# Optimization experiments

Measured on AMD Instinct MI355X. Metric: run time of the kernel, lower is better.

The kernel has to match this reference:

```python
import jax, jax.numpy as jnp
import numpy as np

N_EMBD = 1024
N_HEAD = 16
HEAD_DIM = N_EMBD // N_HEAD


def setup_inputs() -> dict:
    key = jax.random.key(0)
    ks = jax.random.split(key, 5)
    x = jax.random.normal(ks[0], (2, 2048, N_EMBD), dtype=jnp.float32)
    # Linear params, scaled like torch default init (~U(-1/sqrt(fan_in),..)) approximated with small normal
    s = 1.0 / np.sqrt(N_EMBD)
    W_qkv = jax.random.normal(ks[1], (N_EMBD, 3 * N_EMBD), dtype=jnp.float32) * s
    b_qkv = jax.random.normal(ks[2], (3 * N_EMBD,), dtype=jnp.float32) * s
    W_proj = jax.random.normal(ks[3], (N_EMBD, N_EMBD), dtype=jnp.float32) * s
    b_proj = jax.random.normal(ks[4], (N_EMBD,), dtype=jnp.float32) * s
    return {"x": x, "W_qkv": W_qkv, "b_qkv": b_qkv, "W_proj": W_proj, "b_proj": b_proj}


def reference(x, W_qkv, b_qkv, W_proj, b_proj):
    B, T, C = x.shape
    qkv = x @ W_qkv + b_qkv                              # [B,T,3C]
    qkv = qkv.reshape(B, T, 3, N_HEAD, HEAD_DIM)
    qkv = jnp.transpose(qkv, (2, 0, 3, 1, 4))            # [3,B,H,T,D]
    q, k, v = qkv[0], qkv[1], qkv[2]
    scale = HEAD_DIM ** -0.5
    att = jnp.einsum('bhqd,bhkd->bhqk', q, k) * scale    # [B,H,T,T]
    causal = jnp.tril(jnp.ones((T, T), dtype=bool))
    att = jnp.where(causal, att, -jnp.inf)
    att = jax.nn.softmax(att, axis=-1)
    y = jnp.einsum('bhqk,bhkd->bhqd', att, v)            # [B,H,T,D]
    y = jnp.transpose(y, (0, 2, 1, 3)).reshape(B, T, C)
    return y @ W_proj + b_proj
```

## Files before the change

### kernel.cpp

```cpp
#include <hip/hip_runtime.h>
#include <hip/hip_bf16.h>
#include <stdint.h>

#define N_EMBD 1024
#define N_HEAD 16
#define HEAD_DIM 64
#define T_SEQ 2048
#define BATCH 2
#define M_TOK (BATCH * T_SEQ)

typedef short bf16x8 __attribute__((ext_vector_type(8)));
typedef float f32x4 __attribute__((ext_vector_type(4)));

__device__ __forceinline__ void gload_lds16(const void* g, void* l) {
  __builtin_amdgcn_global_load_lds(
      (const __attribute__((address_space(1))) void*)g,
      (__attribute__((address_space(3))) void*)l, 16, 0, 0);
}

__device__ __forceinline__ uint16_t f2bf(float x) {
  uint32_t u = __float_as_uint(x);
  uint32_t r = (u + 0x7FFFu + ((u >> 16) & 1u)) >> 16;
  return (uint16_t)r;
}

__global__ void convert_f32_bf16(const float* __restrict__ in,
                                 uint16_t* __restrict__ out, int n) {
  int i = (blockIdx.x * blockDim.x + threadIdx.x) * 4;
  int stride = gridDim.x * blockDim.x * 4;
  for (; i + 3 < n; i += stride) {
    float4 v = *(const float4*)(in + i);
    ushort4 o;
    o.x = f2bf(v.x); o.y = f2bf(v.y); o.z = f2bf(v.z); o.w = f2bf(v.w);
    *(ushort4*)(out + i) = o;
  }
}

__global__ void transpose_convert(const float* __restrict__ W,
                                  uint16_t* __restrict__ Wt, int R, int C_) {
  __shared__ uint16_t t[64][65];
  int c0 = blockIdx.x * 64, r0 = blockIdx.y * 64;
  int lc = threadIdx.x & 63, lr4 = threadIdx.x >> 6;
#pragma unroll
  for (int rr = 0; rr < 16; ++rr) {
    int r = rr * 4 + lr4;
    t[r][lc] = f2bf(W[(size_t)(r0 + r) * C_ + c0 + lc]);
  }
  __syncthreads();
#pragma unroll
  for (int rr = 0; rr < 16; ++rr) {
    int r = rr * 4 + lr4;
    Wt[(size_t)(c0 + r) * R + r0 + lc] = t[lc][r];
  }
}

__global__ void transpose_v(const uint16_t* __restrict__ qkv,
                            uint16_t* __restrict__ Vt) {
  __shared__ uint16_t t[64][65];
  int t0 = blockIdx.x * 64;
  int bh = blockIdx.y;
  int b = bh >> 4, h = bh & 15;
  int lc = threadIdx.x & 63, lr4 = threadIdx.x >> 6;
  const uint16_t* src =
      qkv + (size_t)(b * T_SEQ) * (3 * N_EMBD) + 2 * N_EMBD + h * 64;
#pragma unroll
  for (int rr = 0; rr < 16; ++rr) {
    int r = rr * 4 + lr4;
    t[r][lc] = src[(size_t)(t0 + r) * (3 * N_EMBD) + lc];
  }
  __syncthreads();
  uint16_t* dst = Vt + (size_t)bh * 64 * T_SEQ;
#pragma unroll
  for (int rr = 0; rr < 16; ++rr) {
    int d = rr * 4 + lr4;
    dst[(size_t)d * T_SEQ + t0 + lc] = t[lc][d];
  }
}

template <int OUT_BF16>
__global__ __launch_bounds__(256) void gemm_bt(
    const uint16_t* __restrict__ A, const uint16_t* __restrict__ Bt,
    const float* __restrict__ bias, void* __restrict__ Cv, int M, int N,
    int K) {
  __shared__ __attribute__((aligned(16))) uint16_t sA[2][128 * 32];
  __shared__ __attribute__((aligned(16))) uint16_t sB[2][128 * 32];
  int tid = threadIdx.x;
  int w = tid >> 6, l = tid & 63;
  int wm = w >> 1, wn = w & 1;
  int ql = l & 15, hi = l >> 4;
  size_t m0 = (size_t)blockIdx.x * 128, n0 = (size_t)blockIdx.y * 128;
  f32x4 acc[4][4] = {};

#pragma unroll
  for (int r = 0; r < 2; ++r) {
    int base = r * 256 + (w << 6);
    int idx = base + l;
    gload_lds16(A + (m0 + (idx >> 2)) * K + (idx & 3) * 8, &sA[0][0] + base * 8);
    gload_lds16(Bt + (n0 + (idx >> 2)) * K + (idx & 3) * 8, &sB[0][0] + base * 8);
  }

  int cur = 0;
  for (int kt = 0; kt < K; kt += 32) {
    if (kt + 32 < K) {
#pragma unroll
      for (int r = 0; r < 2; ++r) {
        int base = r * 256 + (w << 6);
        int idx = base + l;
        gload_lds16(A + (m0 + (idx >> 2)) * K + kt + 32 + (idx & 3) * 8,
                    &sA[cur ^ 1][0] + base * 8);
        gload_lds16(Bt + (n0 + (idx >> 2)) * K + kt + 32 + (idx & 3) * 8,
                    &sB[cur ^ 1][0] + base * 8);
      }
      asm volatile("s_waitcnt vmcnt(4)" ::: "memory");
    } else {
      asm volatile("s_waitcnt vmcnt(0)" ::: "memory");
    }
    __builtin_amdgcn_s_barrier();
    __builtin_amdgcn_sched_barrier(0);
    bf16x8 af[4], bfr[4];
#pragma unroll
    for (int i = 0; i < 4; i++)
      af[i] = *(const bf16x8*)(&sA[cur][0] + (wm * 64 + i * 16 + ql) * 32 + hi * 8);
#pragma unroll
    for (int j = 0; j < 4; j++)
      bfr[j] = *(const bf16x8*)(&sB[cur][0] + (wn * 64 + j * 16 + ql) * 32 + hi * 8);
#pragma unroll
    for (int i = 0; i < 4; i++)
#pragma unroll
      for (int j = 0; j < 4; j++)
        acc[i][j] = __builtin_amdgcn_mfma_f32_16x16x32_bf16(af[i], bfr[j],
                                                            acc[i][j], 0, 0, 0);
    __builtin_amdgcn_sched_barrier(0);
    __builtin_amdgcn_s_barrier();
    cur ^= 1;
  }

#pragma unroll
  for (int i = 0; i < 4; i++) {
    size_t m = m0 + wm * 64 + i * 16 + hi * 4;
#pragma unroll
    for (int j = 0; j < 4; j++) {
      size_t n = n0 + wn * 64 + j * 16 + ql;
      float bv = bias[n];
#pragma unroll
      for (int r = 0; r < 4; r++) {
        float v = acc[i][j][r] + bv;
        if (OUT_BF16)
          ((uint16_t*)Cv)[(m + r) * N + n] = f2bf(v);
        else
          ((float*)Cv)[(m + r) * N + n] = v;
      }
    }
  }
}

__device__ __forceinline__ void sm_pack(const f32x4* sfr, f32x4* acc,
                                        float& m_run, float& l_part, bool mask,
                                        int qloc, int hi, bool lo, int sl0,
                                        int sl1, bf16x8& pf0o, bf16x8& pf1o) {
  float sv[16];
  if (mask) {
    const int kb0 = 4 * hi;
#pragma unroll
    for (int f = 0; f < 4; ++f)
#pragma unroll
      for (int r = 0; r < 4; ++r)
        sv[4 * f + r] = (16 * f + kb0 + r <= qloc) ? sfr[f][r] : -1e30f;
  } else {
#pragma unroll
    for (int f = 0; f < 4; ++f)
#pragma unroll
      for (int r = 0; r < 4; ++r) sv[4 * f + r] = sfr[f][r];
  }
  float x0 = fmaxf(fmaxf(sv[0], sv[1]), fmaxf(sv[2], sv[3]));
  float x1 = fmaxf(fmaxf(sv[4], sv[5]), fmaxf(sv[6], sv[7]));
  float x2 = fmaxf(fmaxf(sv[8], sv[9]), fmaxf(sv[10], sv[11]));
  float x3 = fmaxf(fmaxf(sv[12], sv[13]), fmaxf(sv[14], sv[15]));
  float tmax = fmaxf(fmaxf(x0, x1), fmaxf(x2, x3));
  if (__any(tmax > m_run)) {
    float tm = fmaxf(tmax, __shfl_xor(tmax, 16));
    tm = fmaxf(tm, __shfl_xor(tm, 32));
    float m_new = fmaxf(m_run, tm);
    float corr = __expf(m_run - m_new);
    m_run = m_new;
    l_part *= corr;
#pragma unroll
    for (int d = 0; d < 4; ++d) acc[d] *= corr;
  }
  float pv[16];
#pragma unroll
  for (int i2 = 0; i2 < 16; ++i2) pv[i2] = __expf(sv[i2] - m_run);
  float s01 = (pv[0] + pv[1]) + (pv[2] + pv[3]);
  float s23 = (pv[4] + pv[5]) + (pv[6] + pv[7]);
  float s45 = (pv[8] + pv[9]) + (pv[10] + pv[11]);
  float s67 = (pv[12] + pv[13]) + (pv[14] + pv[15]);
  l_part += (s01 + s23) + (s45 + s67);
  uint32_t wp[8];
#pragma unroll
  for (int f = 0; f < 4; ++f) {
    asm("v_cvt_pk_bf16_f32 %0, %1, %2"
        : "=v"(wp[2 * f]) : "v"(pv[4 * f]), "v"(pv[4 * f + 1]));
    asm("v_cvt_pk_bf16_f32 %0, %1, %2"
        : "=v"(wp[2 * f + 1]) : "v"(pv[4 * f + 2]), "v"(pv[4 * f + 3]));
  }
  union { uint32_t u[4]; bf16x8 v; } pf0, pf1;
  {
    uint32_t a0 = __shfl((int)wp[0], sl0), b0 = __shfl((int)wp[2], sl0);
    uint32_t a1 = __shfl((int)wp[1], sl0), b1 = __shfl((int)wp[3], sl0);
    uint32_t a2 = __shfl((int)wp[0], sl1), b2 = __shfl((int)wp[2], sl1);
    uint32_t a3 = __shfl((int)wp[1], sl1), b3 = __shfl((int)wp[3], sl1);
    pf0.u[0] = lo ? a0 : b0; pf0.u[1] = lo ? a1 : b1;
    pf0.u[2] = lo ? a2 : b2; pf0.u[3] = lo ? a3 : b3;
  }
  {
    uint32_t a0 = __shfl((int)wp[4], sl0), b0 = __shfl((int)wp[6], sl0);
    uint32_t a1 = __shfl((int)wp[5], sl0), b1 = __shfl((int)wp[7], sl0);
    uint32_t a2 = __shfl((int)wp[4], sl1), b2 = __shfl((int)wp[6], sl1);
    uint32_t a3 = __shfl((int)wp[5], sl1), b3 = __shfl((int)wp[7], sl1);
    pf1.u[0] = lo ? a0 : b0; pf1.u[1] = lo ? a1 : b1;
    pf1.u[2] = lo ? a2 : b2; pf1.u[3] = lo ? a3 : b3;
  }
  pf0o = pf0.v;
  pf1o = pf1.v;
}

__device__ __forceinline__ void load_q_scaled(const uint16_t* Qb, int qg,
                                              int hi, bf16x8& q0, bf16x8& q1) {
  const size_t rs = 3 * N_EMBD;
  q0 = *(const bf16x8*)(Qb + (size_t)qg * rs + hi * 8);
  q1 = *(const bf16x8*)(Qb + (size_t)qg * rs + 32 + hi * 8);
#pragma unroll
  for (int j = 0; j < 8; ++j) {
    uint16_t u = (uint16_t)q0[j];
    q0[j] = (short)(((u & 0x7f80u) >= 0x180u) ? (u - 0x180u) : (u & 0x8000u));
    uint16_t v = (uint16_t)q1[j];
    q1[j] = (short)(((v & 0x7f80u) >= 0x180u) ? (v - 0x180u) : (v & 0x8000u));
  }
}

__device__ __forceinline__ void write_o(const f32x4* acc, float l_part,
                                        uint16_t* y, int b, int h, int qg,
                                        int hi) {
  float lt = l_part + __shfl_xor(l_part, 16);
  lt += __shfl_xor(lt, 32);
  float inv = 1.0f / lt;
  uint16_t* yrow = y + (size_t)(b * T_SEQ + qg) * N_EMBD + h * 64;
#pragma unroll
  for (int d = 0; d < 4; ++d) {
    uint32_t o01, o23;
    float v0 = acc[d][0] * inv, v1 = acc[d][1] * inv;
    float v2 = acc[d][2] * inv, v3 = acc[d][3] * inv;
    asm("v_cvt_pk_bf16_f32 %0, %1, %2" : "=v"(o01) : "v"(v0), "v"(v1));
    asm("v_cvt_pk_bf16_f32 %0, %1, %2" : "=v"(o23) : "v"(v2), "v"(v3));
    *(uint32_t*)(yrow + d * 16 + hi * 4) = o01;
    *(uint32_t*)(yrow + d * 16 + hi * 4 + 2) = o23;
  }
}

__global__ __launch_bounds__(256, 2) void attn_kernel(
    const uint16_t* __restrict__ qkv, const uint16_t* __restrict__ Vt,
    uint16_t* __restrict__ y) {
  __shared__ __attribute__((aligned(16))) uint16_t sK[2][64 * 64];
  __shared__ __attribute__((aligned(16))) uint16_t sV[2][64 * 64];

  int tid = threadIdx.x;
  int w = tid >> 6, l = tid & 63;
  int ql = l & 15, hi = l >> 4;
  int id = blockIdx.x;
  int xcd = id & 7;
  int bh = xcd * 4 + ((id >> 3) & 3);
  int qt = 15 - (id >> 5);
  int b = bh >> 4, h = bh & 15;
  const size_t rs = 3 * N_EMBD;
  const uint16_t* Qb = qkv + (size_t)(b * T_SEQ) * rs + h * 64;
  const uint16_t* Kb = Qb + N_EMBD;
  const uint16_t* Vb = Vt + (size_t)bh * 64 * T_SEQ;
  const bool lo = hi < 2;
  const int sl0 = ql + ((hi & 1) << 5);
  const int sl1 = sl0 + 16;
  const int qloc = w * 16 + ql;
  const int qgA = qt * 128 + qloc;
  const int qgB = qgA + 64;

  bf16x8 qfA0, qfA1, qfB0, qfB1;
  load_q_scaled(Qb, qgA, hi, qfA0, qfA1);
  load_q_scaled(Qb, qgB, hi, qfB0, qfB1);

  f32x4 accA[4] = {}, accB[4] = {};
  float mA = -1e30f, lA = 0.f, mB = -1e30f, lB = 0.f;
  const int xr = (ql & 7) * 8;
  const int nIter = 2 * qt + 2;

#pragma unroll
  for (int s2 = 0; s2 < 2; ++s2) {
    int base16 = s2 * 256 + w * 64;
    int idx = base16 + l;
    int row = idx >> 3, c = idx & 7;
    int d8 = c ^ (row & 7);
    gload_lds16(Kb + (size_t)row * rs + d8 * 8, &sK[0][0] + base16 * 8);
    gload_lds16(Vb + (size_t)row * T_SEQ + 0 + d8 * 8, &sV[0][0] + base16 * 8);
  }

  int cur = 0;
  for (int t = 0; t < nIter; ++t) {
    const bool actA = (t <= 2 * qt);
    if (t + 1 < nIter) {
      const int kvn = (t + 1) << 6;
#pragma unroll
      for (int s2 = 0; s2 < 2; ++s2) {
        int base16 = s2 * 256 + w * 64;
        int idx = base16 + l;
        int row = idx >> 3, c = idx & 7;
        int d8 = c ^ (row & 7);
        gload_lds16(Kb + (size_t)(kvn + row) * rs + d8 * 8,
                    &sK[cur ^ 1][0] + base16 * 8);
        gload_lds16(Vb + (size_t)row * T_SEQ + kvn + d8 * 8,
                    &sV[cur ^ 1][0] + base16 * 8);
      }
      asm volatile("s_waitcnt vmcnt(4)" ::: "memory");
    } else {
      asm volatile("s_waitcnt vmcnt(0)" ::: "memory");
    }
    __builtin_amdgcn_s_barrier();
    __builtin_amdgcn_sched_barrier(0);
    const uint16_t* kb_l = &sK[cur][0];
    const uint16_t* vb_l = &sV[cur][0];
    bf16x8 kf[8];
#pragma unroll
    for (int f = 0; f < 4; ++f) {
      kf[2 * f] = *(const bf16x8*)(kb_l + (16 * f + ql) * 64 + ((hi * 8) ^ xr));
      kf[2 * f + 1] =
          *(const bf16x8*)(kb_l + (16 * f + ql) * 64 + (((4 + hi) * 8) ^ xr));
    }
    f32x4 sA[4] = {}, sB[4] = {};
    __builtin_amdgcn_s_setprio(1);
    if (actA) {
#pragma unroll
      for (int f = 0; f < 4; ++f) {
        sA[f] = __builtin_amdgcn_mfma_f32_16x16x32_bf16(kf[2 * f], qfA0, sA[f], 0, 0, 0);
        sA[f] = __builtin_amdgcn_mfma_f32_16x16x32_bf16(kf[2 * f + 1], qfA1, sA[f], 0, 0, 0);
      }
    }
#pragma unroll
    for (int f = 0; f < 4; ++f) {
      sB[f] = __builtin_amdgcn_mfma_f32_16x16x32_bf16(kf[2 * f], qfB0, sB[f], 0, 0, 0);
      sB[f] = __builtin_amdgcn_mfma_f32_16x16x32_bf16(kf[2 * f + 1], qfB1, sB[f], 0, 0, 0);
    }
    __builtin_amdgcn_s_setprio(0);
    bf16x8 vf[8];
#pragma unroll
    for (int d = 0; d < 4; ++d) {
      vf[2 * d] = *(const bf16x8*)(vb_l + (16 * d + ql) * 64 + ((hi * 8) ^ xr));
      vf[2 * d + 1] =
          *(const bf16x8*)(vb_l + (16 * d + ql) * 64 + (((4 + hi) * 8) ^ xr));
    }
    bf16x8 pA0, pA1, pB0, pB1;
    if (actA)
      sm_pack(sA, accA, mA, lA, t == 2 * qt, qloc, hi, lo, sl0, sl1, pA0, pA1);
    sm_pack(sB, accB, mB, lB, t == 2 * qt + 1, qloc, hi, lo, sl0, sl1, pB0, pB1);
    __builtin_amdgcn_s_setprio(1);
    if (actA) {
#pragma unroll
      for (int d = 0; d < 4; ++d)
        accA[d] = __builtin_amdgcn_mfma_f32_16x16x32_bf16(vf[2 * d], pA0, accA[d], 0, 0, 0);
#pragma unroll
      for (int d = 0; d < 4; ++d)
        accA[d] = __builtin_amdgcn_mfma_f32_16x16x32_bf16(vf[2 * d + 1], pA1, accA[d], 0, 0, 0);
    }
#pragma unroll
    for (int d = 0; d < 4; ++d)
      accB[d] = __builtin_amdgcn_mfma_f32_16x16x32_bf16(vf[2 * d], pB0, accB[d], 0, 0, 0);
#pragma unroll
    for (int d = 0; d < 4; ++d)
      accB[d] = __builtin_amdgcn_mfma_f32_16x16x32_bf16(vf[2 * d + 1], pB1, accB[d], 0, 0, 0);
    __builtin_amdgcn_s_setprio(0);
    __builtin_amdgcn_sched_barrier(0);
    __builtin_amdgcn_s_barrier();
    cur ^= 1;
  }

  write_o(accA, lA, y, b, h, qgA, hi);
  write_o(accB, lB, y, b, h, qgB, hi);
}

extern "C" void kernel_launch(void* const* d_in, const int* in_sizes, int n_in,
                              void* d_out, int out_size, void* d_ws,
                              size_t ws_size, hipStream_t stream) {
  const float* x = (const float*)d_in[0];
  const float* Wqkv = (const float*)d_in[1];
  const float* bqkv = (const float*)d_in[2];
  const float* Wproj = (const float*)d_in[3];
  const float* bproj = (const float*)d_in[4];
  float* out = (float*)d_out;

  uint8_t* ws = (uint8_t*)d_ws;
  uint16_t* xb = (uint16_t*)(ws);
  uint16_t* wqkvT = (uint16_t*)(ws + (8u << 20));
  uint16_t* wprojT = (uint16_t*)(ws + (14u << 20));
  uint16_t* qkv = (uint16_t*)(ws + (16u << 20));
  uint16_t* vt = (uint16_t*)(ws + (40u << 20));
  uint16_t* yb = (uint16_t*)(ws + (48u << 20));

  convert_f32_bf16<<<dim3(4096), dim3(256), 0, stream>>>(x, xb,
                                                         M_TOK * N_EMBD);
  transpose_convert<<<dim3(3072 / 64, 1024 / 64), dim3(256), 0, stream>>>(
      Wqkv, wqkvT, 1024, 3072);
  transpose_convert<<<dim3(1024 / 64, 1024 / 64), dim3(256), 0, stream>>>(
      Wproj, wprojT, 1024, 1024);
  gemm_bt<1><<<dim3(M_TOK / 128, 3072 / 128), dim3(256), 0, stream>>>(
      xb, wqkvT, bqkv, qkv, M_TOK, 3072, 1024);
  transpose_v<<<dim3(T_SEQ / 64, 32), dim3(256), 0, stream>>>(qkv, vt);
  attn_kernel<<<dim3(512), dim3(256), 0, stream>>>(qkv, vt, yb);
  gemm_bt<0><<<dim3(M_TOK / 128, 1024 / 128), dim3(256), 0, stream>>>(
      yb, wprojT, bproj, out, M_TOK, 1024, 1024);
}
```

Measured before the change: 138.3 us.

## Split attention into 64-query tiles with 2-wave blocks and double grid

The attention kernel now uses 128-thread blocks (2 waves), each covering a 64-query tile instead of a 128-query tile, and the grid grows from 512 to 1024 blocks. Each wave still handles two 16-row query groups (A and B), but both now share the same diagonal KV tile. This removes the per-iteration actA predicate and interleaves the A and B MFMAs. The aim is more blocks and better causal load balance, at the cost of each block doing more KV loads per thread and KV tiles being reloaded by twice as many blocks.

Result: faster. 135.4 us (-2.0%).

```diff
diff --git a/kernel.cpp b/kernel.cpp
--- a/kernel.cpp
+++ b/kernel.cpp
@@ -257,7 +257,7 @@
   }
 }
 
-__global__ __launch_bounds__(256, 2) void attn_kernel(
+__global__ __launch_bounds__(128, 2) void attn_kernel(
     const uint16_t* __restrict__ qkv, const uint16_t* __restrict__ Vt,
     uint16_t* __restrict__ y) {
   __shared__ __attribute__((aligned(16))) uint16_t sK[2][64 * 64];
@@ -269,7 +269,7 @@
   int id = blockIdx.x;
   int xcd = id & 7;
   int bh = xcd * 4 + ((id >> 3) & 3);
-  int qt = 15 - (id >> 5);
+  int qt = 31 - (id >> 5);
   int b = bh >> 4, h = bh & 15;
   const size_t rs = 3 * N_EMBD;
   const uint16_t* Qb = qkv + (size_t)(b * T_SEQ) * rs + h * 64;
@@ -278,9 +278,10 @@
   const bool lo = hi < 2;
   const int sl0 = ql + ((hi & 1) << 5);
   const int sl1 = sl0 + 16;
-  const int qloc = w * 16 + ql;
-  const int qgA = qt * 128 + qloc;
-  const int qgB = qgA + 64;
+  const int qlocA = w * 16 + ql;
+  const int qlocB = qlocA + 32;
+  const int qgA = qt * 64 + qlocA;
+  const int qgB = qt * 64 + qlocB;
 
   bf16x8 qfA0, qfA1, qfB0, qfB1;
   load_q_scaled(Qb, qgA, hi, qfA0, qfA1);
@@ -289,26 +290,25 @@
   f32x4 accA[4] = {}, accB[4] = {};
   float mA = -1e30f, lA = 0.f, mB = -1e30f, lB = 0.f;
   const int xr = (ql & 7) * 8;
-  const int nIter = 2 * qt + 2;
-
-#pragma unroll
-  for (int s2 = 0; s2 < 2; ++s2) {
-    int base16 = s2 * 256 + w * 64;
+  const int nIter = qt + 1;
+
+#pragma unroll
+  for (int s2 = 0; s2 < 4; ++s2) {
+    int base16 = s2 * 128 + w * 64;
     int idx = base16 + l;
     int row = idx >> 3, c = idx & 7;
     int d8 = c ^ (row & 7);
     gload_lds16(Kb + (size_t)row * rs + d8 * 8, &sK[0][0] + base16 * 8);
-    gload_lds16(Vb + (size_t)row * T_SEQ + 0 + d8 * 8, &sV[0][0] + base16 * 8);
+    gload_lds16(Vb + (size_t)row * T_SEQ + d8 * 8, &sV[0][0] + base16 * 8);
   }
 
   int cur = 0;
   for (int t = 0; t < nIter; ++t) {
-    const bool actA = (t <= 2 * qt);
     if (t + 1 < nIter) {
       const int kvn = (t + 1) << 6;
 #pragma unroll
-      for (int s2 = 0; s2 < 2; ++s2) {
-        int base16 = s2 * 256 + w * 64;
+      for (int s2 = 0; s2 < 4; ++s2) {
+        int base16 = s2 * 128 + w * 64;
         int idx = base16 + l;
         int row = idx >> 3, c = idx & 7;
         int d8 = c ^ (row & 7);
@@ -317,7 +317,7 @@
         gload_lds16(Vb + (size_t)row * T_SEQ + kvn + d8 * 8,
                     &sV[cur ^ 1][0] + base16 * 8);
       }
-      asm volatile("s_waitcnt vmcnt(4)" ::: "memory");
+      asm volatile("s_waitcnt vmcnt(8)" ::: "memory");
     } else {
       asm volatile("s_waitcnt vmcnt(0)" ::: "memory");
     }
@@ -334,15 +334,10 @@
     }
     f32x4 sA[4] = {}, sB[4] = {};
     __builtin_amdgcn_s_setprio(1);
-    if (actA) {
-#pragma unroll
-      for (int f = 0; f < 4; ++f) {
-        sA[f] = __builtin_amdgcn_mfma_f32_16x16x32_bf16(kf[2 * f], qfA0, sA[f], 0, 0, 0);
-        sA[f] = __builtin_amdgcn_mfma_f32_16x16x32_bf16(kf[2 * f + 1], qfA1, sA[f], 0, 0, 0);
-      }
-    }
 #pragma unroll
     for (int f = 0; f < 4; ++f) {
+      sA[f] = __builtin_amdgcn_mfma_f32_16x16x32_bf16(kf[2 * f], qfA0, sA[f], 0, 0, 0);
+      sA[f] = __builtin_amdgcn_mfma_f32_16x16x32_bf16(kf[2 * f + 1], qfA1, sA[f], 0, 0, 0);
       sB[f] = __builtin_amdgcn_mfma_f32_16x16x32_bf16(kf[2 * f], qfB0, sB[f], 0, 0, 0);
       sB[f] = __builtin_amdgcn_mfma_f32_16x16x32_bf16(kf[2 * f + 1], qfB1, sB[f], 0, 0, 0);
     }
@@ -355,24 +350,16 @@
           *(const bf16x8*)(vb_l + (16 * d + ql) * 64 + (((4 + hi) * 8) ^ xr));
     }
     bf16x8 pA0, pA1, pB0, pB1;
-    if (actA)
-      sm_pack(sA, accA, mA, lA, t == 2 * qt, qloc, hi, lo, sl0, sl1, pA0, pA1);
-    sm_pack(sB, accB, mB, lB, t == 2 * qt + 1, qloc, hi, lo, sl0, sl1, pB0, pB1);
+    sm_pack(sA, accA, mA, lA, t == qt, qlocA, hi, lo, sl0, sl1, pA0, pA1);
+    sm_pack(sB, accB, mB, lB, t == qt, qlocB, hi, lo, sl0, sl1, pB0, pB1);
     __builtin_amdgcn_s_setprio(1);
-    if (actA) {
-#pragma unroll
-      for (int d = 0; d < 4; ++d)
-        accA[d] = __builtin_amdgcn_mfma_f32_16x16x32_bf16(vf[2 * d], pA0, accA[d], 0, 0, 0);
-#pragma unroll
-      for (int d = 0; d < 4; ++d)
-        accA[d] = __builtin_amdgcn_mfma_f32_16x16x32_bf16(vf[2 * d + 1], pA1, accA[d], 0, 0, 0);
-    }
-#pragma unroll
-    for (int d = 0; d < 4; ++d)
+#pragma unroll
+    for (int d = 0; d < 4; ++d) {
+      accA[d] = __builtin_amdgcn_mfma_f32_16x16x32_bf16(vf[2 * d], pA0, accA[d], 0, 0, 0);
+      accA[d] = __builtin_amdgcn_mfma_f32_16x16x32_bf16(vf[2 * d + 1], pA1, accA[d], 0, 0, 0);
       accB[d] = __builtin_amdgcn_mfma_f32_16x16x32_bf16(vf[2 * d], pB0, accB[d], 0, 0, 0);
-#pragma unroll
-    for (int d = 0; d < 4; ++d)
       accB[d] = __builtin_amdgcn_mfma_f32_16x16x32_bf16(vf[2 * d + 1], pB1, accB[d], 0, 0, 0);
+    }
     __builtin_amdgcn_s_setprio(0);
     __builtin_amdgcn_sched_barrier(0);
     __builtin_amdgcn_s_barrier();
@@ -410,7 +397,7 @@
   gemm_bt<1><<<dim3(M_TOK / 128, 3072 / 128), dim3(256), 0, stream>>>(
       xb, wqkvT, bqkv, qkv, M_TOK, 3072, 1024);
   transpose_v<<<dim3(T_SEQ / 64, 32), dim3(256), 0, stream>>>(qkv, vt);
-  attn_kernel<<<dim3(512), dim3(256), 0, stream>>>(qkv, vt, yb);
+  attn_kernel<<<dim3(1024), dim3(128), 0, stream>>>(qkv, vt, yb);
   gemm_bt<0><<<dim3(M_TOK / 128, 1024 / 128), dim3(256), 0, stream>>>(
       yb, wprojT, bproj, out, M_TOK, 1024, 1024);
 }
```
